# Kernel optimization log

Hardware: AMD Instinct MI355X
Metric: run time of the kernel (lower is better)

## Reference

```python
import jax, jax.numpy as jnp
import numpy as np

EMB_NUM = 1024
EMB_DIM = 256


def setup_inputs() -> dict:
    key = jax.random.key(0)
    k1, k2 = jax.random.split(key)
    z = jax.random.normal(k1, (64, 32, 32, EMB_DIM), dtype=jnp.float32)
    # nn.Embedding weight initialized uniform(-1/emb_num, 1/emb_num)
    emb = jax.random.uniform(k2, (EMB_NUM, EMB_DIM), dtype=jnp.float32,
                             minval=-1.0 / EMB_NUM, maxval=1.0 / EMB_NUM)
    return {"z": z, "emb": emb}


def reference(z, emb):
    z_shape = z.shape
    flat_z = z.reshape(-1, EMB_DIM)                      # [N, D]
    # squared-distance matrix: ||z||^2 + ||e||^2 - 2 z.e  -> [N, K]
    distance = (jnp.sum(flat_z ** 2, axis=1, keepdims=True)
                + jnp.sum(emb ** 2, axis=1)
                - 2.0 * jnp.matmul(flat_z, emb.T))
    idx = jnp.argmin(distance, axis=1)                   # [N]
    # one-hot @ emb is just a gather of the nearest codebook rows
    quantized_z = jnp.take(emb, idx, axis=0).reshape(z_shape)
    commitment_loss = 0.5 * jnp.mean((jax.lax.stop_gradient(quantized_z) - z) ** 2)
    emb_loss = 0.5 * jnp.mean((quantized_z - jax.lax.stop_gradient(z)) ** 2)
    # straight-through estimator
    quantized_z = z + jax.lax.stop_gradient(quantized_z - z)
    return (quantized_z, commitment_loss, emb_loss)
```

## Files before the change

### kernel.cpp

```cpp
#include <hip/hip_runtime.h>

#define K_CODES 1024
#define DIM     256
#define NROWS   65536
#define THREADS 256
#define ROWS_PER_WAVE 32
#define ROWS_PER_BLOCK 128
#define NBLOCKS (NROWS / ROWS_PER_BLOCK)
#define CHUNK_CODES 32
#define NCHUNK (K_CODES / CHUNK_CODES)
#define CHUNK_BYTES (CHUNK_CODES * DIM * 2)

typedef __attribute__((ext_vector_type(8))) short short8;
typedef __attribute__((ext_vector_type(4))) float f32x4;

__device__ __forceinline__ unsigned short f2bf(float f) {
    unsigned int u = __float_as_uint(f);
    u += 0x7fffu + ((u >> 16) & 1u);
    return (unsigned short)(u >> 16);
}

__device__ __forceinline__ void gload_lds16(const void* g, void* l) {
    __builtin_amdgcn_global_load_lds(
        (const __attribute__((address_space(1))) void*)g,
        (__attribute__((address_space(3))) void*)l, 16, 0, 0);
}

__global__ void k_prep(const float* __restrict__ emb,
                       unsigned short* __restrict__ embb2,
                       float* __restrict__ hneT,
                       float* __restrict__ lossAcc) {
    __shared__ float snormw[8][16];
    const int c   = blockIdx.x;
    const int tid = threadIdx.x;
    const int m   = tid >> 6;
    const int l   = tid & 63;
    const int r   = l & 15;
    const int q   = l >> 4;

    const float* src = emb + (size_t)(c * 16 + r) * DIM + m * 32 + q * 8;
    float4 a = *reinterpret_cast<const float4*>(src);
    float4 b = *reinterpret_cast<const float4*>(src + 4);
    float s = a.x*a.x + a.y*a.y + a.z*a.z + a.w*a.w
            + b.x*b.x + b.y*b.y + b.z*b.z + b.w*b.w;
    short8 sv;
    sv[0]=(short)f2bf(a.x); sv[1]=(short)f2bf(a.y); sv[2]=(short)f2bf(a.z); sv[3]=(short)f2bf(a.w);
    sv[4]=(short)f2bf(b.x); sv[5]=(short)f2bf(b.y); sv[6]=(short)f2bf(b.z); sv[7]=(short)f2bf(b.w);
    reinterpret_cast<short8*>(embb2)[(size_t)(c * 8 + m) * 64 + l] = sv;

    s += __shfl_xor(s, 16, 64);
    s += __shfl_xor(s, 32, 64);
    if (l < 16) snormw[m][l] = s;
    __syncthreads();
    if (tid < 16) {
        float t = 0.f;
        #pragma unroll
        for (int mm = 0; mm < 8; ++mm) t += snormw[mm][tid];
        hneT[c * 16 + tid] = -0.5f * t;
    }
    if (c == 0 && tid == 0) *lossAcc = 0.f;
}

__launch_bounds__(THREADS, 2)
__global__ void k_main(const float* __restrict__ z,
                       const unsigned short* __restrict__ embb2,
                       const float* __restrict__ hneT,
                       const float* __restrict__ emb,
                       float* __restrict__ out,
                       float* __restrict__ lossAcc) {
    __shared__ __align__(16) char ebuf[2][CHUNK_BYTES];

    const int tid  = threadIdx.x;
    const int lane = tid & 63;
    const int w    = tid >> 6;
    const int r    = lane & 15;
    const int q    = lane >> 4;
    const long grow0 = (long)blockIdx.x * ROWS_PER_BLOCK + w * ROWS_PER_WAVE;

    {
        const char* src = reinterpret_cast<const char*>(embb2) + (size_t)tid * 16;
        char* dst = ebuf[0] + tid * 16;
        #pragma unroll
        for (int j = 0; j < 4; ++j)
            gload_lds16(src + j * 4096, dst + j * 4096);
    }

    short8 af[2][8];
    float  zn[2];
    #pragma unroll
    for (int t = 0; t < 2; ++t) {
        const float* zr = z + (grow0 + t * 16 + r) * DIM + q * 8;
        float s = 0.f;
        #pragma unroll
        for (int m = 0; m < 8; ++m) {
            float4 a = *reinterpret_cast<const float4*>(zr + m * 32);
            float4 b = *reinterpret_cast<const float4*>(zr + m * 32 + 4);
            s += a.x*a.x + a.y*a.y + a.z*a.z + a.w*a.w
               + b.x*b.x + b.y*b.y + b.z*b.z + b.w*b.w;
            short8 sv;
            sv[0]=(short)f2bf(a.x); sv[1]=(short)f2bf(a.y); sv[2]=(short)f2bf(a.z); sv[3]=(short)f2bf(a.w);
            sv[4]=(short)f2bf(b.x); sv[5]=(short)f2bf(b.y); sv[6]=(short)f2bf(b.z); sv[7]=(short)f2bf(b.w);
            af[t][m] = sv;
        }
        s += __shfl_xor(s, 16, 64);
        s += __shfl_xor(s, 32, 64);
        zn[t] = s;
    }

    float kb0[4], kb1[4];
    #pragma unroll
    for (int j = 0; j < 4; ++j) { kb0[j] = -1e30f; kb1[j] = -1e30f; }

    __syncthreads();

    for (int c = 0; c < NCHUNK; ++c) {
        const int cur = c & 1;
        if (c + 1 < NCHUNK) {
            const char* src = reinterpret_cast<const char*>(embb2)
                              + (size_t)(c + 1) * CHUNK_BYTES + (size_t)tid * 16;
            char* dst = ebuf[cur ^ 1] + tid * 16;
            #pragma unroll
            for (int j = 0; j < 4; ++j)
                gload_lds16(src + j * 4096, dst + j * 4096);
        }

        const float hne0 = hneT[c * CHUNK_CODES + r];
        const float hne1 = hneT[c * CHUNK_CODES + 16 + r];
        const char* bbase = ebuf[cur] + (size_t)lane * 16;

        #pragma unroll
        for (int g = 0; g < 2; ++g) {
            short8 bf[8];
            #pragma unroll
            for (int m = 0; m < 8; ++m)
                bf[m] = *reinterpret_cast<const short8*>(bbase + (g * 8 + m) * 1024);
            const float hne = (g == 0) ? hne0 : hne1;
            f32x4 a0 = {hne, hne, hne, hne};
            f32x4 a1 = {hne, hne, hne, hne};
            #pragma unroll
            for (int m = 0; m < 8; ++m) {
                a0 = __builtin_amdgcn_mfma_f32_16x16x32_bf16(af[0][m], bf[m], a0, 0, 0, 0);
                a1 = __builtin_amdgcn_mfma_f32_16x16x32_bf16(af[1][m], bf[m], a1, 0, 0, 0);
            }
            const unsigned tag = 1023u - (unsigned)(c * CHUNK_CODES + g * 16 + r);
            #pragma unroll
            for (int j = 0; j < 4; ++j) {
                kb0[j] = fmaxf(kb0[j], __uint_as_float((__float_as_uint(a0[j]) & 0xFFFFFC00u) | tag));
                kb1[j] = fmaxf(kb1[j], __uint_as_float((__float_as_uint(a1[j]) & 0xFFFFFC00u) | tag));
            }
        }
        __syncthreads();
    }

    #pragma unroll
    for (int j = 0; j < 4; ++j) {
        #pragma unroll
        for (int m = 1; m < 16; m <<= 1) {
            kb0[j] = fmaxf(kb0[j], __shfl_xor(kb0[j], m, 64));
            kb1[j] = fmaxf(kb1[j], __shfl_xor(kb1[j], m, 64));
        }
    }

    float lp = 0.f;
    #pragma unroll
    for (int rr = 0; rr < 32; ++rr) {
        const int t = rr >> 4, r16 = rr & 15;
        const int qq = r16 >> 2, rsub = r16 & 3;
        float kv = __shfl((t == 0) ? kb0[rsub] : kb1[rsub], qq * 16, 64);
        const unsigned ku = __float_as_uint(kv);
        const int   code  = 1023 - (int)(ku & 1023u);
        const float score = __uint_as_float(ku & 0xFFFFFC00u);
        float4 v = *reinterpret_cast<const float4*>(emb + (size_t)code * DIM + lane * 4);
        *reinterpret_cast<float4*>(out + (size_t)(grow0 + rr) * DIM + lane * 4) = v;
        float zr = __shfl(zn[t], r16, 64);
        lp += zr - 2.f * score;
    }
    if (lane == 0) atomicAdd(lossAcc, lp);
}

__global__ void k_loss(const float* __restrict__ lossAcc, float* __restrict__ out2) {
    float loss = 0.5f * lossAcc[0] * (1.f / 16777216.f);
    out2[0] = loss;
    out2[1] = loss;
}

extern "C" void kernel_launch(void* const* d_in, const int* in_sizes, int n_in,
                              void* d_out, int out_size, void* d_ws, size_t ws_size,
                              hipStream_t stream) {
    const float* z   = (const float*)d_in[0];
    const float* emb = (const float*)d_in[1];
    float* out = (float*)d_out;
    char*  ws  = (char*)d_ws;
    float* lossAcc        = (float*)ws;
    float* hneT           = (float*)(ws + 256);
    unsigned short* embb2 = (unsigned short*)(ws + 256 + 4096);

    k_prep<<<K_CODES / 16, 512, 0, stream>>>(emb, embb2, hneT, lossAcc);
    k_main<<<NBLOCKS, THREADS, 0, stream>>>(z, embb2, hneT, emb, out, lossAcc);
    k_loss<<<1, 1, 0, stream>>>(lossAcc, out + (long)NROWS * DIM);
}
```

Measured before the change: 163.4 us.

## Halve rows per wave, raise occupancy, split MFMA chains, stage norms in LDS

Each wave now handles 16 rows instead of 32. The block covers 64 rows, so twice as many blocks are launched, and launch bounds allow 4 blocks per CU. Each 8-step MFMA accumulation is split into two independent 4-step chains that are summed afterwards, and the per-code norms are staged in LDS. Loss partials are reduced per block before one atomic. The aim is more occupancy and latency hiding, traded against each embedding chunk in LDS being reused by half as many rows, which doubles total codebook traffic from L2 to LDS.

```diff
diff --git a/kernel.cpp b/kernel.cpp
--- a/kernel.cpp
+++ b/kernel.cpp
@@ -4,8 +4,8 @@
 #define DIM     256
 #define NROWS   65536
 #define THREADS 256
-#define ROWS_PER_WAVE 32
-#define ROWS_PER_BLOCK 128
+#define ROWS_PER_WAVE 16
+#define ROWS_PER_BLOCK 64
 #define NBLOCKS (NROWS / ROWS_PER_BLOCK)
 #define CHUNK_CODES 32
 #define NCHUNK (K_CODES / CHUNK_CODES)
@@ -61,7 +61,7 @@
     if (c == 0 && tid == 0) *lossAcc = 0.f;
 }
 
-__launch_bounds__(THREADS, 2)
+__launch_bounds__(THREADS, 4)
 __global__ void k_main(const float* __restrict__ z,
                        const unsigned short* __restrict__ embb2,
                        const float* __restrict__ hneT,
@@ -69,6 +69,8 @@
                        float* __restrict__ out,
                        float* __restrict__ lossAcc) {
     __shared__ __align__(16) char ebuf[2][CHUNK_BYTES];
+    __shared__ float shne[K_CODES];
+    __shared__ float swsum[4];
 
     const int tid  = threadIdx.x;
     const int lane = tid & 63;
@@ -84,12 +86,14 @@
         for (int j = 0; j < 4; ++j)
             gload_lds16(src + j * 4096, dst + j * 4096);
     }
-
-    short8 af[2][8];
-    float  zn[2];
-    #pragma unroll
-    for (int t = 0; t < 2; ++t) {
-        const float* zr = z + (grow0 + t * 16 + r) * DIM + q * 8;
+    #pragma unroll
+    for (int i = 0; i < K_CODES / THREADS; ++i)
+        shne[i * THREADS + tid] = hneT[i * THREADS + tid];
+
+    short8 af[8];
+    float  zn;
+    {
+        const float* zr = z + (grow0 + r) * DIM + q * 8;
         float s = 0.f;
         #pragma unroll
         for (int m = 0; m < 8; ++m) {
@@ -100,16 +104,16 @@
             short8 sv;
             sv[0]=(short)f2bf(a.x); sv[1]=(short)f2bf(a.y); sv[2]=(short)f2bf(a.z); sv[3]=(short)f2bf(a.w);
             sv[4]=(short)f2bf(b.x); sv[5]=(short)f2bf(b.y); sv[6]=(short)f2bf(b.z); sv[7]=(short)f2bf(b.w);
-            af[t][m] = sv;
+            af[m] = sv;
         }
         s += __shfl_xor(s, 16, 64);
         s += __shfl_xor(s, 32, 64);
-        zn[t] = s;
-    }
-
-    float kb0[4], kb1[4];
-    #pragma unroll
-    for (int j = 0; j < 4; ++j) { kb0[j] = -1e30f; kb1[j] = -1e30f; }
+        zn = s;
+    }
+
+    float kb[4];
+    #pragma unroll
+    for (int j = 0; j < 4; ++j) kb[j] = -1e30f;
 
     __syncthreads();
 
@@ -124,8 +128,8 @@
                 gload_lds16(src + j * 4096, dst + j * 4096);
         }
 
-        const float hne0 = hneT[c * CHUNK_CODES + r];
-        const float hne1 = hneT[c * CHUNK_CODES + 16 + r];
+        const float hne0 = shne[c * CHUNK_CODES + r];
+        const float hne1 = shne[c * CHUNK_CODES + 16 + r];
         const char* bbase = ebuf[cur] + (size_t)lane * 16;
 
         #pragma unroll
@@ -134,19 +138,19 @@
             #pragma unroll
             for (int m = 0; m < 8; ++m)
                 bf[m] = *reinterpret_cast<const short8*>(bbase + (g * 8 + m) * 1024);
+            f32x4 alo = {0.f, 0.f, 0.f, 0.f};
+            f32x4 ahi = {0.f, 0.f, 0.f, 0.f};
+            #pragma unroll
+            for (int m = 0; m < 4; ++m) {
+                alo = __builtin_amdgcn_mfma_f32_16x16x32_bf16(af[m],     bf[m],     alo, 0, 0, 0);
+                ahi = __builtin_amdgcn_mfma_f32_16x16x32_bf16(af[m + 4], bf[m + 4], ahi, 0, 0, 0);
+            }
             const float hne = (g == 0) ? hne0 : hne1;
-            f32x4 a0 = {hne, hne, hne, hne};
-            f32x4 a1 = {hne, hne, hne, hne};
-            #pragma unroll
-            for (int m = 0; m < 8; ++m) {
-                a0 = __builtin_amdgcn_mfma_f32_16x16x32_bf16(af[0][m], bf[m], a0, 0, 0, 0);
-                a1 = __builtin_amdgcn_mfma_f32_16x16x32_bf16(af[1][m], bf[m], a1, 0, 0, 0);
-            }
             const unsigned tag = 1023u - (unsigned)(c * CHUNK_CODES + g * 16 + r);
             #pragma unroll
             for (int j = 0; j < 4; ++j) {
-                kb0[j] = fmaxf(kb0[j], __uint_as_float((__float_as_uint(a0[j]) & 0xFFFFFC00u) | tag));
-                kb1[j] = fmaxf(kb1[j], __uint_as_float((__float_as_uint(a1[j]) & 0xFFFFFC00u) | tag));
+                float sc = alo[j] + ahi[j] + hne;
+                kb[j] = fmaxf(kb[j], __uint_as_float((__float_as_uint(sc) & 0xFFFFFC00u) | tag));
             }
         }
         __syncthreads();
@@ -155,27 +159,27 @@
     #pragma unroll
     for (int j = 0; j < 4; ++j) {
         #pragma unroll
-        for (int m = 1; m < 16; m <<= 1) {
-            kb0[j] = fmaxf(kb0[j], __shfl_xor(kb0[j], m, 64));
-            kb1[j] = fmaxf(kb1[j], __shfl_xor(kb1[j], m, 64));
-        }
+        for (int m = 1; m < 16; m <<= 1)
+            kb[j] = fmaxf(kb[j], __shfl_xor(kb[j], m, 64));
     }
 
     float lp = 0.f;
     #pragma unroll
-    for (int rr = 0; rr < 32; ++rr) {
-        const int t = rr >> 4, r16 = rr & 15;
-        const int qq = r16 >> 2, rsub = r16 & 3;
-        float kv = __shfl((t == 0) ? kb0[rsub] : kb1[rsub], qq * 16, 64);
+    for (int rr = 0; rr < 16; ++rr) {
+        const int qq = rr >> 2, j = rr & 3;
+        float kv = __shfl(kb[j], qq * 16, 64);
         const unsigned ku = __float_as_uint(kv);
         const int   code  = 1023 - (int)(ku & 1023u);
         const float score = __uint_as_float(ku & 0xFFFFFC00u);
         float4 v = *reinterpret_cast<const float4*>(emb + (size_t)code * DIM + lane * 4);
         *reinterpret_cast<float4*>(out + (size_t)(grow0 + rr) * DIM + lane * 4) = v;
-        float zr = __shfl(zn[t], r16, 64);
+        float zr = __shfl(zn, rr, 64);
         lp += zr - 2.f * score;
     }
-    if (lane == 0) atomicAdd(lossAcc, lp);
+    if (lane == 0) swsum[w] = lp;
+    __syncthreads();
+    if (tid == 0)
+        atomicAdd(lossAcc, swsum[0] + swsum[1] + swsum[2] + swsum[3]);
 }
 
 __global__ void k_loss(const float* __restrict__ lossAcc, float* __restrict__ out2) {
```

After: 155.0 us. 1.05x faster.
